# Kernel tuning notes

Hardware: AMD Instinct MI355X
Metric: run time of the kernel (lower is better)

The kernel has to match this reference:

```python
import jax, jax.numpy as jnp
import numpy as np
import math

B, T, E, H = 4, 4096, 1024, 16
D = E // H  # head dim
EPS_DENOM = 1e-6
LN_EPS = 1e-5


def setup_inputs() -> dict:
    key = jax.random.key(0)
    ks = jax.random.split(key, 8)
    s = 0.02
    return {
        "x": jax.random.normal(ks[0], (B, T, E), jnp.float32),
        "ln1_w": jnp.ones((E,), jnp.float32),
        "ln1_b": jnp.zeros((E,), jnp.float32),
        "wq": jax.random.normal(ks[1], (E, E), jnp.float32) * s,
        "bq": jnp.zeros((E,), jnp.float32),
        "wk": jax.random.normal(ks[2], (E, E), jnp.float32) * s,
        "bk": jnp.zeros((E,), jnp.float32),
        "wv": jax.random.normal(ks[3], (E, E), jnp.float32) * s,
        "bv": jnp.zeros((E,), jnp.float32),
        "wo": jax.random.normal(ks[4], (E, E), jnp.float32) * s,
        "bo": jnp.zeros((E,), jnp.float32),
        "ln2_w": jnp.ones((E,), jnp.float32),
        "ln2_b": jnp.zeros((E,), jnp.float32),
        "w_fc": jax.random.normal(ks[5], (E, 4 * E), jnp.float32) * s,
        "b_fc": jnp.zeros((4 * E,), jnp.float32),
        "w_proj": jax.random.normal(ks[6], (4 * E, E), jnp.float32) * s,
        "b_proj": jnp.zeros((E,), jnp.float32),
    }


def _layernorm(x, w, b):
    mu = jnp.mean(x, axis=-1, keepdims=True)
    var = jnp.mean(jnp.square(x - mu), axis=-1, keepdims=True)
    return (x - mu) * jax.lax.rsqrt(var + LN_EPS) * w + b


def _cosformer_attn(x, wq, bq, wk, bk, wv, bv, wo, bo):
    # ReLU feature map on q, k projections
    q = jax.nn.relu(x @ wq + bq)  # [B,T,E]
    k = jax.nn.relu(x @ wk + bk)
    v = x @ wv + bv
    # split heads -> [B,H,T,D]
    q = q.reshape(B, T, H, D).transpose(0, 2, 1, 3)
    k = k.reshape(B, T, H, D).transpose(0, 2, 1, 3)
    v = v.reshape(B, T, H, D).transpose(0, 2, 1, 3)
    # cosine reweighting: idx_i = pi/2 * (i+1)/M, M = T (self-attention)
    idx = (math.pi / 2.0) * jnp.arange(1, T + 1, dtype=x.dtype) / T  # [T]
    s = jnp.sin(idx)[None, None, :, None]
    c = jnp.cos(idx)[None, None, :, None]
    q_ = jnp.concatenate([q * s, q * c], axis=-1)  # [B,H,T,2D]
    k_ = jnp.concatenate([k * s, k * c], axis=-1)  # [B,H,T,2D]
    # non-causal linear attention: O = Q' (K'^T V) / (Q' K'^T 1)
    kv = jnp.einsum("bhtd,bhte->bhde", k_, v)       # [B,H,2D,D]
    z = 1.0 / jnp.maximum(jnp.einsum("bhtd,bhd->bht", q_, k_.sum(axis=2)), EPS_DENOM)
    out = jnp.einsum("bhtd,bhde,bht->bhte", q_, kv, z)  # [B,H,T,D]
    out = out.transpose(0, 2, 1, 3).reshape(B, T, E)
    return out @ wo + bo


def reference(x, ln1_w, ln1_b, wq, bq, wk, bk, wv, bv, wo, bo,
              ln2_w, ln2_b, w_fc, b_fc, w_proj, b_proj):
    h = _layernorm(x, ln1_w, ln1_b)
    x = x + _cosformer_attn(h, wq, bq, wk, bk, wv, bv, wo, bo)
    h = _layernorm(x, ln2_w, ln2_b)
    h = jax.nn.gelu(h @ w_fc + b_fc, approximate=False) @ w_proj + b_proj
    return x + h
```

## Files before the change

### kernel.cpp

```cpp
#include <hip/hip_runtime.h>

#define PI_F 3.14159265358979f
#define MT 16384
#define EE 1024
#define FF 4096
#define NCH 8
#define CHT (4096 / NCH)

typedef unsigned short u16;
typedef __attribute__((ext_vector_type(8))) short short8;
typedef __attribute__((ext_vector_type(4))) float f32x4;

__device__ __forceinline__ float bf2f(u16 u) {
  unsigned int v = ((unsigned int)u) << 16;
  float f;
  __builtin_memcpy(&f, &v, 4);
  return f;
}
__device__ __forceinline__ u16 f2bf(float f) {
  unsigned int x;
  __builtin_memcpy(&x, &f, 4);
  unsigned int r = x + 0x7fffu + ((x >> 16) & 1u);
  return (u16)(r >> 16);
}
__device__ __forceinline__ float ldin(const void* p, long i, int f32) {
  return f32 ? ((const float*)p)[i] : bf2f(((const u16*)p)[i]);
}
__device__ __forceinline__ void async16(const u16* g, u16* l) {
  __builtin_amdgcn_global_load_lds(
      (const __attribute__((address_space(1))) unsigned int*)g,
      (__attribute__((address_space(3))) unsigned int*)l, 16, 0, 0);
}

__global__ __launch_bounds__(256) void detect_dtype(const u16* __restrict__ x,
                                                    int* __restrict__ flag) {
  const int tid = threadIdx.x;
  int cnt = 0;
  for (int i = tid; i < 2048; i += 256) {
    const int e = (x[i] >> 7) & 0xFF;
    if (e == 0 || e >= 0x90) cnt++;
  }
#pragma unroll
  for (int o = 32; o > 0; o >>= 1) cnt += __shfl_xor(cnt, o);
  __shared__ int s[4];
  if ((tid & 63) == 0) s[tid >> 6] = cnt;
  __syncthreads();
  if (tid == 0) flag[0] = (s[0] + s[1] + s[2] + s[3] > 200) ? 1 : 0;
}

__global__ __launch_bounds__(256) void transpose_in(
    const void* __restrict__ src, const int* __restrict__ flag,
    u16* __restrict__ dst, int R, int C) {
  __shared__ float tile[64][65];
  const int f = *flag;
  const int tx = threadIdx.x & 63, ty = threadIdx.x >> 6;
  const long c0 = (long)blockIdx.x * 64, r0 = (long)blockIdx.y * 64;
#pragma unroll
  for (int i = 0; i < 16; i++) {
    const int r = ty + i * 4;
    tile[r][tx] = ldin(src, (r0 + r) * (long)C + c0 + tx, f);
  }
  __syncthreads();
#pragma unroll
  for (int i = 0; i < 16; i++) {
    const int cc = ty + i * 4;
    dst[(c0 + cc) * (long)R + r0 + tx] = f2bf(tile[tx][cc]);
  }
}

__global__ __launch_bounds__(256) void ln_kernel(
    const void* __restrict__ xin, int xmode, const int* __restrict__ flag,
    const void* __restrict__ w, const void* __restrict__ b,
    u16* __restrict__ out) {
  const long row = blockIdx.x;
  const int tid = threadIdx.x;
  const int fl = *flag;
  const int xf = (xmode == 2) ? fl : xmode;
  float v[4];
  if (xf) {
    const float4 q = ((const float4*)((const float*)xin + row * EE))[tid];
    v[0] = q.x; v[1] = q.y; v[2] = q.z; v[3] = q.w;
  } else {
    const ushort4 u = ((const ushort4*)((const u16*)xin + row * EE))[tid];
    v[0] = bf2f(u.x); v[1] = bf2f(u.y); v[2] = bf2f(u.z); v[3] = bf2f(u.w);
  }
  float sum = v[0] + v[1] + v[2] + v[3];
  float sq = v[0] * v[0] + v[1] * v[1] + v[2] * v[2] + v[3] * v[3];
#pragma unroll
  for (int o = 32; o > 0; o >>= 1) {
    sum += __shfl_xor(sum, o);
    sq += __shfl_xor(sq, o);
  }
  __shared__ float s1[4], s2[4];
  const int wave = tid >> 6, lane = tid & 63;
  if (lane == 0) { s1[wave] = sum; s2[wave] = sq; }
  __syncthreads();
  sum = s1[0] + s1[1] + s1[2] + s1[3];
  sq = s2[0] + s2[1] + s2[2] + s2[3];
  const float mu = sum * (1.f / EE);
  const float var = sq * (1.f / EE) - mu * mu;
  const float rs = rsqrtf(var + 1e-5f);
  ushort4 o4;
  float r0 = (v[0] - mu) * rs * ldin(w, tid * 4 + 0, fl) + ldin(b, tid * 4 + 0, fl);
  float r1 = (v[1] - mu) * rs * ldin(w, tid * 4 + 1, fl) + ldin(b, tid * 4 + 1, fl);
  float r2 = (v[2] - mu) * rs * ldin(w, tid * 4 + 2, fl) + ldin(b, tid * 4 + 2, fl);
  float r3 = (v[3] - mu) * rs * ldin(w, tid * 4 + 3, fl) + ldin(b, tid * 4 + 3, fl);
  o4.x = f2bf(r0); o4.y = f2bf(r1); o4.z = f2bf(r2); o4.w = f2bf(r3);
  ((ushort4*)(out + row * EE))[tid] = o4;
}

__global__ __launch_bounds__(256) void gemm_bf16(
    const u16* __restrict__ A, const u16* __restrict__ Bt,
    const void* __restrict__ bias, const void* __restrict__ res, int resMode,
    void* __restrict__ Cout, int outMode, long coff,
    const int* __restrict__ flag, int M, int N, int K, int act) {
  __shared__ u16 As[128 * 32];
  __shared__ u16 Bs[128 * 32];
  const int tid = threadIdx.x;
  const int lane = tid & 63;
  const int wave = tid >> 6;
  const int quad = lane >> 4;
  const int l16 = lane & 15;
  const int wm = (wave >> 1) * 64;
  const int wn = (wave & 1) * 64;
  const long bm = (long)blockIdx.x * 128;
  const long bn = (long)blockIdx.y * 128;

  f32x4 acc[4][4];
#pragma unroll
  for (int i = 0; i < 4; i++)
#pragma unroll
    for (int j = 0; j < 4; j++)
#pragma unroll
      for (int r = 0; r < 4; r++) acc[i][j][r] = 0.f;

  const int srow = tid >> 2;
  const int scol = (tid & 3) * 8;
  const u16* Ap = A + (bm + srow) * (long)K + scol;
  const u16* Bp = Bt + (bn + srow) * (long)K + scol;
  const long K64 = (long)64 * K;
  u16* AsW = As + wave * 512;
  u16* BsW = Bs + wave * 512;

  for (int kt = 0; kt < K; kt += 32) {
    async16(Ap, AsW);
    async16(Ap + K64, AsW + 2048);
    async16(Bp, BsW);
    async16(Bp + K64, BsW + 2048);
    Ap += 32;
    Bp += 32;
    __syncthreads();
    short8 af[4], bfr[4];
#pragma unroll
    for (int i = 0; i < 4; i++)
      af[i] = *(const short8*)&As[(wm + i * 16 + l16) * 32 + quad * 8];
#pragma unroll
    for (int i = 0; i < 4; i++)
      bfr[i] = *(const short8*)&Bs[(wn + i * 16 + l16) * 32 + quad * 8];
#pragma unroll
    for (int mi = 0; mi < 4; mi++)
#pragma unroll
      for (int ni = 0; ni < 4; ni++)
        acc[mi][ni] = __builtin_amdgcn_mfma_f32_16x16x32_bf16(
            af[mi], bfr[ni], acc[mi][ni], 0, 0, 0);
    __syncthreads();
  }

  const int fl = *flag;
  const int outF32 = (outMode == 2) ? fl : outMode;
#pragma unroll
  for (int ni = 0; ni < 4; ni++) {
    const long gc = bn + wn + ni * 16 + l16;
    const float bvv = ldin(bias, gc, fl);
#pragma unroll
    for (int mi = 0; mi < 4; mi++) {
      const long gr0 = bm + wm + mi * 16 + quad * 4;
#pragma unroll
      for (int r = 0; r < 4; r++) {
        float val = acc[mi][ni][r] + bvv;
        if (act == 1) val = fmaxf(val, 0.f);
        else if (act == 2) val = 0.5f * val * (1.f + erff(val * 0.70710678118654752f));
        const long idx = (gr0 + r) * (long)N + gc;
        if (resMode == 1) val += ((const float*)res)[idx];
        else if (resMode == 2) val += ldin(res, idx, fl);
        if (outF32) ((float*)Cout)[coff + idx] = val;
        else ((u16*)Cout)[coff + idx] = f2bf(val);
      }
    }
  }
}

__global__ __launch_bounds__(256) void kv_partial(
    const u16* __restrict__ k, const u16* __restrict__ v,
    float* __restrict__ kvpart, float* __restrict__ kspart) {
  const int bh = blockIdx.x;
  const int ch = blockIdx.y;
  const int b = bh >> 4, h = bh & 15;
  const int tid = threadIdx.x;
  __shared__ float kl[8][64], vl[8][64];
  const int dkq = tid >> 4;
  const int dvq = tid & 15;
  float accS[4][4] = {}, accC[4][4] = {};
  float ksS[4] = {}, ksC[4] = {};
  const int tt = tid >> 5;
  const int cc = (tid & 31) * 2;
  const long base = ((long)b * 4096 + ch * CHT) * EE + h * 64;
  for (int tb = 0; tb < CHT; tb += 8) {
    const long roff = base + (long)(tb + tt) * EE + cc;
    const unsigned int ku = *(const unsigned int*)(k + roff);
    const unsigned int vu = *(const unsigned int*)(v + roff);
    __syncthreads();
    kl[tt][cc] = bf2f((u16)ku);
    kl[tt][cc + 1] = bf2f((u16)(ku >> 16));
    vl[tt][cc] = bf2f((u16)vu);
    vl[tt][cc + 1] = bf2f((u16)(vu >> 16));
    __syncthreads();
#pragma unroll
    for (int j = 0; j < 8; j++) {
      const int t = ch * CHT + tb + j;
      float s, c;
      __sincosf((float)(t + 1) * (PI_F * 0.5f / 4096.f), &s, &c);
      float kk[4], vv[4];
#pragma unroll
      for (int i = 0; i < 4; i++) {
        kk[i] = kl[j][dkq * 4 + i];
        vv[i] = vl[j][dvq * 4 + i];
      }
#pragma unroll
      for (int i = 0; i < 4; i++) {
        const float ks_ = kk[i] * s, kc_ = kk[i] * c;
        ksS[i] += ks_;
        ksC[i] += kc_;
#pragma unroll
        for (int jj = 0; jj < 4; jj++) {
          accS[i][jj] += ks_ * vv[jj];
          accC[i][jj] += kc_ * vv[jj];
        }
      }
    }
  }
  float* outS = kvpart + (((long)ch * 64 + bh) * 2 + 0) * 4096;
  float* outC = outS + 4096;
#pragma unroll
  for (int i = 0; i < 4; i++)
#pragma unroll
    for (int jj = 0; jj < 4; jj++) {
      outS[(dkq * 4 + i) * 64 + dvq * 4 + jj] = accS[i][jj];
      outC[(dkq * 4 + i) * 64 + dvq * 4 + jj] = accC[i][jj];
    }
  if (dvq == 0) {
    float* oS = kspart + ((long)ch * 64 + bh) * 2 * 64;
#pragma unroll
    for (int i = 0; i < 4; i++) {
      oS[dkq * 4 + i] = ksS[i];
      oS[64 + dkq * 4 + i] = ksC[i];
    }
  }
}

__global__ __launch_bounds__(256) void kv_reduce(
    const float* __restrict__ kvpart, const float* __restrict__ kspart,
    float* __restrict__ kvcomb, float* __restrict__ kscomb) {
  const long KVTOT = 64L * 2 * 4096;
  const long KSTOT = 64L * 2 * 64;
  const long idx = (long)blockIdx.x * 256 + threadIdx.x;
  if (idx < KVTOT) {
    float s = 0.f;
#pragma unroll
    for (int chn = 0; chn < NCH; chn++) s += kvpart[chn * KVTOT + idx];
    kvcomb[idx] = s;
  } else {
    const long i2 = idx - KVTOT;
    if (i2 < KSTOT) {
      float s = 0.f;
#pragma unroll
      for (int chn = 0; chn < NCH; chn++) s += kspart[chn * KSTOT + i2];
      kscomb[i2] = s;
    }
  }
}

__global__ __launch_bounds__(256) void attn_apply(
    const u16* __restrict__ q, const float* __restrict__ kvcomb,
    const float* __restrict__ kscomb, u16* __restrict__ attn) {
  const int bh = blockIdx.x;
  const int b = bh >> 4, h = bh & 15;
  const int t0 = blockIdx.y * 64;
  const int tid = threadIdx.x;
  __shared__ float kvl[2][64][64];
  __shared__ float ksl[2][64];
  __shared__ float ql[64][66];

  const float4* kvsrc = (const float4*)(kvcomb + (long)bh * 8192);
  float4* kvdst = (float4*)&kvl[0][0][0];
#pragma unroll
  for (int i = 0; i < 8; i++) kvdst[tid + 256 * i] = kvsrc[tid + 256 * i];
  if (tid < 32) ((float4*)&ksl[0][0])[tid] = ((const float4*)(kscomb + (long)bh * 128))[tid];
  {
    const int r = tid >> 2;
    const int c = (tid & 3) * 16;
    const u16* qp = q + ((long)b * 4096 + t0 + r) * EE + h * 64 + c;
    const uint4 u0 = *(const uint4*)qp;
    const uint4 u1 = *(const uint4*)(qp + 8);
    unsigned int uu[8] = {u0.x, u0.y, u0.z, u0.w, u1.x, u1.y, u1.z, u1.w};
#pragma unroll
    for (int i = 0; i < 8; i++) {
      ql[r][c + 2 * i] = bf2f((u16)uu[i]);
      ql[r][c + 2 * i + 1] = bf2f((u16)(uu[i] >> 16));
    }
  }
  __syncthreads();

  const int tg = tid >> 4;
  const int dvq = tid & 15;
  const int dv0 = dvq * 4;

  float o1[4][4] = {}, o2[4][4] = {}, zs[4] = {}, zc[4] = {};
  for (int dk = 0; dk < 64; dk++) {
    const float ks0 = ksl[0][dk], ks1 = ksl[1][dk];
    float kv0[4], kv1[4];
#pragma unroll
    for (int j = 0; j < 4; j++) {
      kv0[j] = kvl[0][dk][dv0 + j];
      kv1[j] = kvl[1][dk][dv0 + j];
    }
#pragma unroll
    for (int it = 0; it < 4; it++) {
      const float qv = ql[tg + it * 16][dk];
      zs[it] += qv * ks0;
      zc[it] += qv * ks1;
#pragma unroll
      for (int j = 0; j < 4; j++) {
        o1[it][j] += qv * kv0[j];
        o2[it][j] += qv * kv1[j];
      }
    }
  }
#pragma unroll
  for (int it = 0; it < 4; it++) {
    const int t = t0 + tg + it * 16;
    float s, c;
    __sincosf((float)(t + 1) * (PI_F * 0.5f / 4096.f), &s, &c);
    const float z = s * zs[it] + c * zc[it];
    const float zinv = 1.f / fmaxf(z, 1e-6f);
    ushort4 o4;
    o4.x = f2bf((s * o1[it][0] + c * o2[it][0]) * zinv);
    o4.y = f2bf((s * o1[it][1] + c * o2[it][1]) * zinv);
    o4.z = f2bf((s * o1[it][2] + c * o2[it][2]) * zinv);
    o4.w = f2bf((s * o1[it][3] + c * o2[it][3]) * zinv);
    *(ushort4*)(attn + ((long)b * 4096 + t) * EE + h * 64 + dv0) = o4;
  }
}

extern "C" void kernel_launch(void* const* d_in, const int* in_sizes, int n_in,
                              void* d_out, int out_size, void* d_ws, size_t ws_size,
                              hipStream_t stream) {
  const void* x = d_in[0];
  const void* ln1w = d_in[1];
  const void* ln1b = d_in[2];
  const void* wq = d_in[3];
  const void* bq = d_in[4];
  const void* wk = d_in[5];
  const void* bk = d_in[6];
  const void* wv = d_in[7];
  const void* bv = d_in[8];
  const void* wo = d_in[9];
  const void* bo = d_in[10];
  const void* ln2w = d_in[11];
  const void* ln2b = d_in[12];
  const void* wfc = d_in[13];
  const void* bfc = d_in[14];
  const void* wproj = d_in[15];
  const void* bproj = d_in[16];

  char* ws = (char*)d_ws;
  size_t off = 0;
  auto alloc = [&](size_t bytes) -> char* {
    char* p = ws + off;
    off += (bytes + 255) & ~((size_t)255);
    return p;
  };
  int* flag = (int*)alloc(256);
  u16* wqT = (u16*)alloc((size_t)EE * EE * 2);
  u16* wkT = (u16*)alloc((size_t)EE * EE * 2);
  u16* wvT = (u16*)alloc((size_t)EE * EE * 2);
  u16* woT = (u16*)alloc((size_t)EE * EE * 2);
  u16* wfcT = (u16*)alloc((size_t)EE * FF * 2);
  u16* wprojT = (u16*)alloc((size_t)FF * EE * 2);
  u16* h = (u16*)alloc((size_t)MT * EE * 2);
  float* x2 = (float*)alloc((size_t)MT * EE * 4);
  u16* kb = (u16*)alloc((size_t)MT * EE * 2);
  u16* vb = (u16*)alloc((size_t)MT * EE * 2);
  float* kvpart = (float*)alloc((size_t)NCH * 64 * 2 * 64 * 64 * 4);
  float* kspart = (float*)alloc((size_t)NCH * 64 * 2 * 64 * 4);
  float* kvcomb = (float*)alloc((size_t)64 * 2 * 64 * 64 * 4);
  float* kscomb = (float*)alloc((size_t)64 * 2 * 64 * 4);
  u16* qb = kb;
  u16* attnb = vb;
  u16* g = kb;
  (void)ws_size; (void)in_sizes; (void)n_in; (void)out_size;

  detect_dtype<<<1, 256, 0, stream>>>((const u16*)x, flag);

  transpose_in<<<dim3(16, 16), 256, 0, stream>>>(wq, flag, wqT, EE, EE);
  transpose_in<<<dim3(16, 16), 256, 0, stream>>>(wk, flag, wkT, EE, EE);
  transpose_in<<<dim3(16, 16), 256, 0, stream>>>(wv, flag, wvT, EE, EE);
  transpose_in<<<dim3(16, 16), 256, 0, stream>>>(wo, flag, woT, EE, EE);
  transpose_in<<<dim3(64, 16), 256, 0, stream>>>(wfc, flag, wfcT, EE, FF);
  transpose_in<<<dim3(16, 64), 256, 0, stream>>>(wproj, flag, wprojT, FF, EE);

  ln_kernel<<<MT, 256, 0, stream>>>(x, 2, flag, ln1w, ln1b, h);

  gemm_bf16<<<dim3(128, 8), 256, 0, stream>>>(h, wkT, bk, nullptr, 0, kb, 0, 0, flag, MT, EE, EE, 1);
  gemm_bf16<<<dim3(128, 8), 256, 0, stream>>>(h, wvT, bv, nullptr, 0, vb, 0, 0, flag, MT, EE, EE, 0);

  kv_partial<<<dim3(64, NCH), 256, 0, stream>>>(kb, vb, kvpart, kspart);
  kv_reduce<<<2080, 256, 0, stream>>>(kvpart, kspart, kvcomb, kscomb);

  gemm_bf16<<<dim3(128, 8), 256, 0, stream>>>(h, wqT, bq, nullptr, 0, qb, 0, 0, flag, MT, EE, EE, 1);
  attn_apply<<<dim3(64, 64), 256, 0, stream>>>(qb, kvcomb, kscomb, attnb);

  gemm_bf16<<<dim3(128, 8), 256, 0, stream>>>(attnb, woT, bo, x, 2, x2, 1, 0, flag, MT, EE, EE, 0);
  ln_kernel<<<MT, 256, 0, stream>>>(x2, 1, flag, ln2w, ln2b, h);

  for (int c = 0; c < 2; c++) {
    const long ro = (long)c * 8192 * EE;
    gemm_bf16<<<dim3(64, 32), 256, 0, stream>>>(h + ro, wfcT, bfc, nullptr, 0, g, 0, 0, flag,
                                                8192, FF, EE, 2);
    gemm_bf16<<<dim3(64, 8), 256, 0, stream>>>(g, wprojT, bproj, x2 + ro, 1, d_out, 2, ro, flag,
                                               8192, EE, FF, 0);
  }
}
```

Before: 1.313 ms.

## Double-buffer GEMM LDS tiles and fuse Q/K/V projections into one GEMM

The GEMM kernel now uses two LDS buffers, so the async global-to-LDS loads for the next K-tile are issued before the MFMA work on the current tile, and only one barrier is needed per iteration. The three Q/K/V projection GEMMs become a single N=3072 GEMM over concatenated transposed weights and biases, with an epilogue that routes each 1024-column plane to its own buffer and applies ReLU only to the Q and K columns. This cuts launches and re-reads of the LayerNorm output, at the cost of doubled LDS use per block and V being stored in the x2 region until x2 is later overwritten.

```diff
diff --git a/kernel.cpp b/kernel.cpp
--- a/kernel.cpp
+++ b/kernel.cpp
@@ -66,6 +66,17 @@
     const int cc = ty + i * 4;
     dst[(c0 + cc) * (long)R + r0 + tx] = f2bf(tile[tx][cc]);
   }
+}
+
+__global__ __launch_bounds__(256) void concat3(
+    const void* __restrict__ a, const void* __restrict__ b,
+    const void* __restrict__ c, const int* __restrict__ flag,
+    float* __restrict__ out) {
+  const int i = blockIdx.x * 256 + threadIdx.x;
+  const int fl = *flag;
+  if (i < 1024) out[i] = ldin(a, i, fl);
+  else if (i < 2048) out[i] = ldin(b, i - 1024, fl);
+  else if (i < 3072) out[i] = ldin(c, i - 2048, fl);
 }
 
 __global__ __launch_bounds__(256) void ln_kernel(
@@ -111,11 +122,12 @@
 
 __global__ __launch_bounds__(256) void gemm_bf16(
     const u16* __restrict__ A, const u16* __restrict__ Bt,
-    const void* __restrict__ bias, const void* __restrict__ res, int resMode,
-    void* __restrict__ Cout, int outMode, long coff,
+    const void* __restrict__ bias, int biasF32,
+    const void* __restrict__ res, int resMode,
+    void* __restrict__ Cout, void* __restrict__ Cv, int outMode, long coff,
     const int* __restrict__ flag, int M, int N, int K, int act) {
-  __shared__ u16 As[128 * 32];
-  __shared__ u16 Bs[128 * 32];
+  __shared__ u16 As[2][128 * 32];
+  __shared__ u16 Bs[2][128 * 32];
   const int tid = threadIdx.x;
   const int lane = tid & 63;
   const int wave = tid >> 6;
@@ -139,52 +151,76 @@
   const u16* Ap = A + (bm + srow) * (long)K + scol;
   const u16* Bp = Bt + (bn + srow) * (long)K + scol;
   const long K64 = (long)64 * K;
-  u16* AsW = As + wave * 512;
-  u16* BsW = Bs + wave * 512;
-
-  for (int kt = 0; kt < K; kt += 32) {
-    async16(Ap, AsW);
-    async16(Ap + K64, AsW + 2048);
-    async16(Bp, BsW);
-    async16(Bp + K64, BsW + 2048);
+  u16* As0 = &As[0][0];
+  u16* Bs0 = &Bs[0][0];
+
+  auto stage = [&](int b) {
+    u16* Ad = As0 + b * 4096 + wave * 512;
+    u16* Bd = Bs0 + b * 4096 + wave * 512;
+    async16(Ap, Ad);
+    async16(Ap + K64, Ad + 2048);
+    async16(Bp, Bd);
+    async16(Bp + K64, Bd + 2048);
     Ap += 32;
     Bp += 32;
-    __syncthreads();
+  };
+  auto compute = [&](int b) {
+    const u16* Ab = As0 + b * 4096;
+    const u16* Bb = Bs0 + b * 4096;
     short8 af[4], bfr[4];
 #pragma unroll
     for (int i = 0; i < 4; i++)
-      af[i] = *(const short8*)&As[(wm + i * 16 + l16) * 32 + quad * 8];
+      af[i] = *(const short8*)&Ab[(wm + i * 16 + l16) * 32 + quad * 8];
 #pragma unroll
     for (int i = 0; i < 4; i++)
-      bfr[i] = *(const short8*)&Bs[(wn + i * 16 + l16) * 32 + quad * 8];
+      bfr[i] = *(const short8*)&Bb[(wn + i * 16 + l16) * 32 + quad * 8];
 #pragma unroll
     for (int mi = 0; mi < 4; mi++)
 #pragma unroll
       for (int ni = 0; ni < 4; ni++)
         acc[mi][ni] = __builtin_amdgcn_mfma_f32_16x16x32_bf16(
             af[mi], bfr[ni], acc[mi][ni], 0, 0, 0);
+  };
+
+  stage(0);
+  __syncthreads();
+  const int nk = K >> 5;
+  int buf = 0;
+  for (int t = 1; t < nk; t++) {
+    stage(buf ^ 1);
+    compute(buf);
     __syncthreads();
-  }
+    buf ^= 1;
+  }
+  compute(buf);
 
   const int fl = *flag;
-  const int outF32 = (outMode == 2) ? fl : outMode;
 #pragma unroll
   for (int ni = 0; ni < 4; ni++) {
     const long gc = bn + wn + ni * 16 + l16;
-    const float bvv = ldin(bias, gc, fl);
+    const float bvv = biasF32 ? ((const float*)bias)[gc] : ldin(bias, gc, fl);
 #pragma unroll
     for (int mi = 0; mi < 4; mi++) {
       const long gr0 = bm + wm + mi * 16 + quad * 4;
 #pragma unroll
       for (int r = 0; r < 4; r++) {
         float val = acc[mi][ni][r] + bvv;
-        if (act == 1) val = fmaxf(val, 0.f);
+        if (act == 1 || (act == 3 && gc < 2048)) val = fmaxf(val, 0.f);
         else if (act == 2) val = 0.5f * val * (1.f + erff(val * 0.70710678118654752f));
-        const long idx = (gr0 + r) * (long)N + gc;
-        if (resMode == 1) val += ((const float*)res)[idx];
-        else if (resMode == 2) val += ldin(res, idx, fl);
-        if (outF32) ((float*)Cout)[coff + idx] = val;
-        else ((u16*)Cout)[coff + idx] = f2bf(val);
+        const long row = gr0 + r;
+        if (outMode == 3) {
+          const long plane = gc >> 10;
+          u16* dst = (plane == 2) ? (u16*)Cv
+                                  : ((u16*)Cout + plane * ((long)M << 10));
+          dst[(row << 10) + (gc & 1023)] = f2bf(val);
+        } else {
+          const long idx = row * (long)N + gc;
+          float v2 = val;
+          if (resMode == 1) v2 += ((const float*)res)[idx];
+          else if (resMode == 2) v2 += ldin(res, idx, fl);
+          if (outMode == 1 || (outMode == 2 && fl)) ((float*)Cout)[coff + idx] = v2;
+          else ((u16*)Cout)[coff + idx] = f2bf(v2);
+        }
       }
     }
   }
@@ -381,53 +417,54 @@
     return p;
   };
   int* flag = (int*)alloc(256);
-  u16* wqT = (u16*)alloc((size_t)EE * EE * 2);
-  u16* wkT = (u16*)alloc((size_t)EE * EE * 2);
-  u16* wvT = (u16*)alloc((size_t)EE * EE * 2);
+  u16* wqkvT = (u16*)alloc((size_t)3 * EE * EE * 2);
   u16* woT = (u16*)alloc((size_t)EE * EE * 2);
   u16* wfcT = (u16*)alloc((size_t)EE * FF * 2);
   u16* wprojT = (u16*)alloc((size_t)FF * EE * 2);
+  float* qkvBias = (float*)alloc(3072 * 4);
   u16* h = (u16*)alloc((size_t)MT * EE * 2);
   float* x2 = (float*)alloc((size_t)MT * EE * 4);
-  u16* kb = (u16*)alloc((size_t)MT * EE * 2);
-  u16* vb = (u16*)alloc((size_t)MT * EE * 2);
+  u16* qk2 = (u16*)alloc((size_t)2 * MT * EE * 2);
   float* kvpart = (float*)alloc((size_t)NCH * 64 * 2 * 64 * 64 * 4);
   float* kspart = (float*)alloc((size_t)NCH * 64 * 2 * 64 * 4);
   float* kvcomb = (float*)alloc((size_t)64 * 2 * 64 * 64 * 4);
   float* kscomb = (float*)alloc((size_t)64 * 2 * 64 * 4);
-  u16* qb = kb;
-  u16* attnb = vb;
-  u16* g = kb;
+  const long PL = (long)MT * EE;
+  u16* qb = qk2;
+  u16* kb = qk2 + PL;
+  u16* vb = (u16*)x2;
+  u16* attnb = kb;
+  u16* g = qk2;
   (void)ws_size; (void)in_sizes; (void)n_in; (void)out_size;
 
   detect_dtype<<<1, 256, 0, stream>>>((const u16*)x, flag);
 
-  transpose_in<<<dim3(16, 16), 256, 0, stream>>>(wq, flag, wqT, EE, EE);
-  transpose_in<<<dim3(16, 16), 256, 0, stream>>>(wk, flag, wkT, EE, EE);
-  transpose_in<<<dim3(16, 16), 256, 0, stream>>>(wv, flag, wvT, EE, EE);
+  transpose_in<<<dim3(16, 16), 256, 0, stream>>>(wq, flag, wqkvT, EE, EE);
+  transpose_in<<<dim3(16, 16), 256, 0, stream>>>(wk, flag, wqkvT + (size_t)EE * EE, EE, EE);
+  transpose_in<<<dim3(16, 16), 256, 0, stream>>>(wv, flag, wqkvT + (size_t)2 * EE * EE, EE, EE);
   transpose_in<<<dim3(16, 16), 256, 0, stream>>>(wo, flag, woT, EE, EE);
   transpose_in<<<dim3(64, 16), 256, 0, stream>>>(wfc, flag, wfcT, EE, FF);
   transpose_in<<<dim3(16, 64), 256, 0, stream>>>(wproj, flag, wprojT, FF, EE);
+  concat3<<<12, 256, 0, stream>>>(bq, bk, bv, flag, qkvBias);
 
   ln_kernel<<<MT, 256, 0, stream>>>(x, 2, flag, ln1w, ln1b, h);
 
-  gemm_bf16<<<dim3(128, 8), 256, 0, stream>>>(h, wkT, bk, nullptr, 0, kb, 0, 0, flag, MT, EE, EE, 1);
-  gemm_bf16<<<dim3(128, 8), 256, 0, stream>>>(h, wvT, bv, nullptr, 0, vb, 0, 0, flag, MT, EE, EE, 0);
+  gemm_bf16<<<dim3(128, 24), 256, 0, stream>>>(h, wqkvT, qkvBias, 1, nullptr, 0,
+                                               qk2, vb, 3, 0, flag, MT, 3072, EE, 3);
 
   kv_partial<<<dim3(64, NCH), 256, 0, stream>>>(kb, vb, kvpart, kspart);
   kv_reduce<<<2080, 256, 0, stream>>>(kvpart, kspart, kvcomb, kscomb);
-
-  gemm_bf16<<<dim3(128, 8), 256, 0, stream>>>(h, wqT, bq, nullptr, 0, qb, 0, 0, flag, MT, EE, EE, 1);
   attn_apply<<<dim3(64, 64), 256, 0, stream>>>(qb, kvcomb, kscomb, attnb);
 
-  gemm_bf16<<<dim3(128, 8), 256, 0, stream>>>(attnb, woT, bo, x, 2, x2, 1, 0, flag, MT, EE, EE, 0);
+  gemm_bf16<<<dim3(128, 8), 256, 0, stream>>>(attnb, woT, bo, 0, x, 2, x2, nullptr,
+                                              1, 0, flag, MT, EE, EE, 0);
   ln_kernel<<<MT, 256, 0, stream>>>(x2, 1, flag, ln2w, ln2b, h);
 
   for (int c = 0; c < 2; c++) {
     const long ro = (long)c * 8192 * EE;
-    gemm_bf16<<<dim3(64, 32), 256, 0, stream>>>(h + ro, wfcT, bfc, nullptr, 0, g, 0, 0, flag,
-                                                8192, FF, EE, 2);
-    gemm_bf16<<<dim3(64, 8), 256, 0, stream>>>(g, wprojT, bproj, x2 + ro, 1, d_out, 2, ro, flag,
-                                               8192, EE, FF, 0);
-  }
-}
+    gemm_bf16<<<dim3(64, 32), 256, 0, stream>>>(h + ro, wfcT, bfc, 0, nullptr, 0,
+                                                g, nullptr, 0, 0, flag, 8192, FF, EE, 2);
+    gemm_bf16<<<dim3(64, 8), 256, 0, stream>>>(g, wprojT, bproj, 0, x2 + ro, 1,
+                                               d_out, nullptr, 2, ro, flag, 8192, EE, FF, 0);
+  }
+}
```

Result: no change. 1.290 ms (-1.8%).
